# Optimization experiments

Hardware: AMD Instinct MI355X
Metric: run time of the kernel (lower is better)

## Reference

```python
import jax, jax.numpy as jnp
import numpy as np

# Dimensions: input_capsules=output_capsules=2048, slot_size=64, capsule_size=256
# slots_per_core = ceil(256/64) = 4, patch_size = (8,8) so h*w == slot_size
CI, CO, SLOT, SPC, H, W = 2048, 2048, 64, 4, 8, 8
PROBA = 0.1   # connection_probability
EPS = 1e-6    # flax nnx.LayerNorm default epsilon


def setup_inputs() -> dict:
    key = jax.random.key(0)
    k1, k2, k3 = jax.random.split(key, 3)
    x = jax.random.normal(k1, (CI, SPC, H, W), jnp.float32)
    # Wi: glorot_normal as in nnx initializers.glorot_normal()
    Wi = jax.nn.initializers.glorot_normal()(k2, (CI, SLOT, SLOT, SPC, SPC), jnp.float32)
    # LayerNorm params over the fully-flattened vector (input_capsules*capsule_size)
    ln_scale = jnp.ones((CI * SPC * SLOT,), jnp.float32)
    ln_bias = jnp.zeros((CI * SPC * SLOT,), jnp.float32)
    # Co: random sparse binary routing tensor (fast_scrramble), Bernoulli(proba)
    Co = jax.random.bernoulli(k3, PROBA, (CI, SPC, CO, SPC)).astype(jnp.float32)
    return {"x": x, "Wi": Wi, "ln_scale": ln_scale, "ln_bias": ln_bias, "Co": Co}


def reference(x, Wi, ln_scale, ln_bias, Co):
    ci, p, h, w = x.shape
    xr = x.reshape(ci, p, h * w)                      # 'ci p1 h w -> ci p1 (h w)'
    # per-capsule block matmul: 'ijklm, imk -> ilj'
    y = jnp.einsum('ijklm,imk->ilj', Wi, xr)          # (ci, spc, slot)
    y = jax.nn.gelu(y)                                # nnx.gelu (approximate tanh)
    shp = y.shape
    yf = y.reshape(-1)
    mu = jnp.mean(yf)
    var = jnp.var(yf)
    yf = (yf - mu) * jax.lax.rsqrt(var + EPS) * ln_scale + ln_bias  # global LayerNorm
    y = yf.reshape(shp)
    # sparse random-routing mixing: 'ijkl, ijm -> klm'
    out = jnp.einsum('ijkl,ijm->klm', Co, y)          # (co, spc, slot)
    return out.reshape(out.shape[0], out.shape[1], h, w)
```

## Files before the change

kernel.cpp:

```cpp
#include <hip/hip_runtime.h>
#include <hip/hip_bf16.h>

#define CI 2048
#define CO_N 2048
#define SLOT 64
#define SPC 4
#define NELEM (CI*SPC*SLOT)
#define CAP 256
#define IJ (CI*SPC)
#define S_SPLIT 8
#define NC 32

typedef __attribute__((ext_vector_type(8))) short short8;
typedef __attribute__((ext_vector_type(4))) short short4v;
typedef __attribute__((ext_vector_type(4))) float float4v;

union ABFrag { short4v h[2]; short8 v; };

__device__ __forceinline__ unsigned short f2bf(float f) {
    __hip_bfloat16 h = __float2bfloat16(f);
    return __builtin_bit_cast(unsigned short, h);
}

__device__ __forceinline__ float gelu_tanh(float x) {
    const float c0 = 0.7978845608028654f;
    float x3 = x * x * x;
    float t = tanhf(c0 * (x + 0.044715f * x3));
    return 0.5f * x * (1.0f + t);
}

__global__ __launch_bounds__(256) void k1_capsule_mm(
    const float* __restrict__ x, const float* __restrict__ Wi,
    float* __restrict__ y, float* __restrict__ psum, float* __restrict__ psumsq)
{
    __shared__ float xs[CAP];
    __shared__ float part[4][4][SLOT];
    __shared__ float ws_s[4], ws_q[4];
    const int i = blockIdx.x;
    const int t = threadIdx.x;
    xs[t] = x[(size_t)i * CAP + t];
    __syncthreads();

    const int k = t >> 2;
    const int w = t >> 6;
    const float xk0 = xs[k], xk1 = xs[64 + k], xk2 = xs[128 + k], xk3 = xs[192 + k];
    const float4* W4 = (const float4*)Wi + (size_t)i * 16384 + t;

    #pragma unroll 8
    for (int j = 0; j < SLOT; ++j) {
        float4 wv = W4[(size_t)j * 256];
        float p = wv.x * xk0 + wv.y * xk1 + wv.z * xk2 + wv.w * xk3;
        p += __shfl_xor(p, 4);
        p += __shfl_xor(p, 8);
        p += __shfl_xor(p, 16);
        p += __shfl_xor(p, 32);
        if ((t & 63) < 4) part[w][t & 63][j] = p;
    }
    __syncthreads();

    const int l2 = t >> 6, j2 = t & 63;
    float v = part[0][l2][j2] + part[1][l2][j2] + part[2][l2][j2] + part[3][l2][j2];
    float g = gelu_tanh(v);
    y[(size_t)i * CAP + t] = g;

    float s = g, q = g * g;
    #pragma unroll
    for (int off = 32; off > 0; off >>= 1) {
        s += __shfl_down(s, off);
        q += __shfl_down(q, off);
    }
    if ((t & 63) == 0) { ws_s[w] = s; ws_q[w] = q; }
    __syncthreads();
    if (t == 0) {
        psum[i]   = ws_s[0] + ws_s[1] + ws_s[2] + ws_s[3];
        psumsq[i] = ws_q[0] + ws_q[1] + ws_q[2] + ws_q[3];
    }
}

__global__ __launch_bounds__(256) void k2_stats(
    const float* __restrict__ psum, const float* __restrict__ psumsq,
    float* __restrict__ stats)
{
    __shared__ float as[4], aq[4];
    const int t = threadIdx.x;
    float s = 0.f, q = 0.f;
    for (int b = t; b < CI; b += 256) { s += psum[b]; q += psumsq[b]; }
    #pragma unroll
    for (int off = 32; off > 0; off >>= 1) {
        s += __shfl_down(s, off);
        q += __shfl_down(q, off);
    }
    if ((t & 63) == 0) { as[t >> 6] = s; aq[t >> 6] = q; }
    __syncthreads();
    if (t == 0) {
        float S = as[0] + as[1] + as[2] + as[3];
        float Q = aq[0] + aq[1] + aq[2] + aq[3];
        float mu = S / (float)NELEM;
        float var = Q / (float)NELEM - mu * mu;
        stats[0] = mu;
        stats[1] = rsqrtf(var + 1e-6f);
    }
}

__global__ __launch_bounds__(256) void k3_norm_t(
    const float* __restrict__ y, const float* __restrict__ scale,
    const float* __restrict__ bias, const float* __restrict__ stats,
    unsigned short* __restrict__ ynT)
{
    const int c = blockIdx.x;
    const int t = threadIdx.x;
    const float mu = stats[0], inv = stats[1];
    const int base = c * 2048 + t * 8;
    float4 ya = *(const float4*)(y + base);
    float4 yb = *(const float4*)(y + base + 4);
    float4 sa = *(const float4*)(scale + base);
    float4 sb = *(const float4*)(scale + base + 4);
    float4 ba = *(const float4*)(bias + base);
    float4 bb = *(const float4*)(bias + base + 4);
    const int ij = c * 32 + (t >> 3);
    const int m0 = (t & 7) * 8;
    float v[8] = { (ya.x-mu)*inv*sa.x+ba.x, (ya.y-mu)*inv*sa.y+ba.y,
                   (ya.z-mu)*inv*sa.z+ba.z, (ya.w-mu)*inv*sa.w+ba.w,
                   (yb.x-mu)*inv*sb.x+bb.x, (yb.y-mu)*inv*sb.y+bb.y,
                   (yb.z-mu)*inv*sb.z+bb.z, (yb.w-mu)*inv*sb.w+bb.w };
    #pragma unroll
    for (int e = 0; e < 8; ++e)
        ynT[(size_t)(m0 + e) * IJ + ij] = f2bf(v[e]);
}

__global__ __launch_bounds__(256) void k4_route_mfma(
    const float* __restrict__ Co, const unsigned short* __restrict__ ynT,
    float* __restrict__ out, float* __restrict__ partial, int use_partial)
{
    __shared__ unsigned short lds_a[64 * 36];
    const int t    = threadIdx.x;
    const int kb   = blockIdx.x;
    const int pc   = blockIdx.y;
    const int klb  = kb * 64;
    const int w    = t >> 6;
    const int lane = t & 63;
    const int quad = lane >> 4;
    const int n16  = lane & 15;

    const int p  = t >> 4;
    const int c4 = (t & 15) * 4;

    const float* co_base = Co + ((size_t)(pc * 1024 + 2 * p)) * IJ + klb + c4;
    const unsigned short* ynT_base = ynT + (size_t)(pc * 1024) + quad * 8;

    float4v acc[4];
    #pragma unroll
    for (int mt = 0; mt < 4; ++mt) acc[mt] = (float4v)(0.f);

    float4 co0 = *(const float4*)(co_base);
    float4 co1 = *(const float4*)(co_base + IJ);

    for (int g = 0; g < NC; ++g) {
        __syncthreads();
        unsigned int* lw = (unsigned int*)lds_a;
        lw[(c4 + 0) * 18 + p] = (unsigned int)f2bf(co0.x) | ((unsigned int)f2bf(co1.x) << 16);
        lw[(c4 + 1) * 18 + p] = (unsigned int)f2bf(co0.y) | ((unsigned int)f2bf(co1.y) << 16);
        lw[(c4 + 2) * 18 + p] = (unsigned int)f2bf(co0.z) | ((unsigned int)f2bf(co1.z) << 16);
        lw[(c4 + 3) * 18 + p] = (unsigned int)f2bf(co0.w) | ((unsigned int)f2bf(co1.w) << 16);
        __syncthreads();
        if (g + 1 < NC) {
            const float* nb = co_base + (size_t)(g + 1) * 32 * IJ;
            co0 = *(const float4*)(nb);
            co1 = *(const float4*)(nb + IJ);
        }
        const unsigned short* arow = lds_a + (w * 16 + n16) * 36 + quad * 8;
        ABFrag af;
        af.h[0] = *(const short4v*)(arow);
        af.h[1] = *(const short4v*)(arow + 4);
        const unsigned short* yb = ynT_base + (size_t)g * 32;
        #pragma unroll
        for (int mt = 0; mt < 4; ++mt) {
            short8 bf = *(const short8*)(yb + (size_t)(mt * 16 + n16) * IJ);
            acc[mt] = __builtin_amdgcn_mfma_f32_16x16x32_bf16(af.v, bf, acc[mt], 0, 0, 0);
        }
    }

    if (use_partial) {
        float* pp = partial + (size_t)pc * NELEM;
        #pragma unroll
        for (int mt = 0; mt < 4; ++mt)
            #pragma unroll
            for (int r = 0; r < 4; ++r)
                pp[(size_t)(klb + w * 16 + quad * 4 + r) * 64 + mt * 16 + n16] = acc[mt][r];
    } else {
        #pragma unroll
        for (int mt = 0; mt < 4; ++mt)
            #pragma unroll
            for (int r = 0; r < 4; ++r)
                atomicAdd(out + (size_t)(klb + w * 16 + quad * 4 + r) * 64 + mt * 16 + n16, acc[mt][r]);
    }
}

__global__ __launch_bounds__(256) void k5_reduce(
    const float* __restrict__ partial, float* __restrict__ out)
{
    const int idx = blockIdx.x * 256 + threadIdx.x;
    float s = 0.f;
    #pragma unroll
    for (int pcs = 0; pcs < S_SPLIT; ++pcs) s += partial[(size_t)pcs * NELEM + idx];
    out[idx] = s;
}

extern "C" void kernel_launch(void* const* d_in, const int* in_sizes, int n_in,
                              void* d_out, int out_size, void* d_ws, size_t ws_size,
                              hipStream_t stream) {
    const float* x        = (const float*)d_in[0];
    const float* Wi       = (const float*)d_in[1];
    const float* ln_scale = (const float*)d_in[2];
    const float* ln_bias  = (const float*)d_in[3];
    const float* Co       = (const float*)d_in[4];
    float* out = (float*)d_out;

    float* ws = (float*)d_ws;
    float* y      = ws;
    float* psum   = y + NELEM;
    float* psumsq = psum + CI;
    float* stats  = psumsq + CI;
    unsigned short* ynT = (unsigned short*)(ws + 528392);
    float* partial = ws + 790536;

    const int use_partial = (ws_size >= (size_t)(790536 + S_SPLIT * NELEM) * sizeof(float)) ? 1 : 0;

    k1_capsule_mm<<<CI, 256, 0, stream>>>(x, Wi, y, psum, psumsq);
    k2_stats<<<1, 256, 0, stream>>>(psum, psumsq, stats);
    k3_norm_t<<<256, 256, 0, stream>>>(y, ln_scale, ln_bias, stats, ynT);
    if (!use_partial)
        hipMemsetAsync(out, 0, (size_t)out_size * sizeof(float), stream);
    k4_route_mfma<<<dim3(128, S_SPLIT), 256, 0, stream>>>(Co, ynT, out, partial, use_partial);
    if (use_partial)
        k5_reduce<<<NELEM / 256, 256, 0, stream>>>(partial, out);
}
```

Before: 877.0 us.

## Fuse stats into norm kernel, restructure capsule matmul, double-buffer routing MFMA

Folds the single-block stats kernel into the normalize/transpose kernel, so every block recomputes the global mean and variance from the partial sums and one launch is removed. The capsule matmul is rewritten so each thread owns one output and loops over k with a transposed x in LDS, replacing the shuffle reductions and cross-wave combine. The routing MFMA kernel double-buffers its LDS tile, dropping one barrier per iteration, and prefetches the next B fragments into registers. Trade-offs: the Wi reads are now strided per thread (1024 floats between threads), which may hurt coalescing, and register pressure rises in the MFMA loop.

After: 873.0 us. No clear change (-0.5%).

```diff
diff --git a/kernel.cpp b/kernel.cpp
--- a/kernel.cpp
+++ b/kernel.cpp
@@ -34,34 +34,27 @@
     float* __restrict__ y, float* __restrict__ psum, float* __restrict__ psumsq)
 {
     __shared__ float xs[CAP];
-    __shared__ float part[4][4][SLOT];
     __shared__ float ws_s[4], ws_q[4];
     const int i = blockIdx.x;
     const int t = threadIdx.x;
-    xs[t] = x[(size_t)i * CAP + t];
-    __syncthreads();
-
-    const int k = t >> 2;
-    const int w = t >> 6;
-    const float xk0 = xs[k], xk1 = xs[64 + k], xk2 = xs[128 + k], xk3 = xs[192 + k];
-    const float4* W4 = (const float4*)Wi + (size_t)i * 16384 + t;
-
+    {
+        const int m = t >> 6, k = t & 63;
+        xs[k * 4 + m] = x[(size_t)i * CAP + t];
+    }
+    __syncthreads();
+
+    const int j = t >> 2;
+    const int l = t & 3;
+    const float* Wb = Wi + (size_t)i * 65536 + j * 1024 + l * 4;
+    float p = 0.f;
     #pragma unroll 8
-    for (int j = 0; j < SLOT; ++j) {
-        float4 wv = W4[(size_t)j * 256];
-        float p = wv.x * xk0 + wv.y * xk1 + wv.z * xk2 + wv.w * xk3;
-        p += __shfl_xor(p, 4);
-        p += __shfl_xor(p, 8);
-        p += __shfl_xor(p, 16);
-        p += __shfl_xor(p, 32);
-        if ((t & 63) < 4) part[w][t & 63][j] = p;
-    }
-    __syncthreads();
-
-    const int l2 = t >> 6, j2 = t & 63;
-    float v = part[0][l2][j2] + part[1][l2][j2] + part[2][l2][j2] + part[3][l2][j2];
-    float g = gelu_tanh(v);
-    y[(size_t)i * CAP + t] = g;
+    for (int k = 0; k < 64; ++k) {
+        float4 wv = *(const float4*)(Wb + k * 16);
+        float4 xv = *(const float4*)(xs + k * 4);
+        p += wv.x * xv.x + wv.y * xv.y + wv.z * xv.z + wv.w * xv.w;
+    }
+    float g = gelu_tanh(p);
+    y[(size_t)i * CAP + l * 64 + j] = g;
 
     float s = g, q = g * g;
     #pragma unroll
@@ -69,6 +62,7 @@
         s += __shfl_down(s, off);
         q += __shfl_down(q, off);
     }
+    const int w = t >> 6;
     if ((t & 63) == 0) { ws_s[w] = s; ws_q[w] = q; }
     __syncthreads();
     if (t == 0) {
@@ -77,13 +71,18 @@
     }
 }
 
-__global__ __launch_bounds__(256) void k2_stats(
-    const float* __restrict__ psum, const float* __restrict__ psumsq,
-    float* __restrict__ stats)
+__global__ __launch_bounds__(256) void k3_norm_t(
+    const float* __restrict__ y, const float* __restrict__ scale,
+    const float* __restrict__ bias, const float* __restrict__ psum,
+    const float* __restrict__ psumsq, unsigned short* __restrict__ ynT)
 {
     __shared__ float as[4], aq[4];
+    __shared__ float sh_mu, sh_inv;
+    const int c = blockIdx.x;
     const int t = threadIdx.x;
+
     float s = 0.f, q = 0.f;
+    #pragma unroll
     for (int b = t; b < CI; b += 256) { s += psum[b]; q += psumsq[b]; }
     #pragma unroll
     for (int off = 32; off > 0; off >>= 1) {
@@ -97,19 +96,12 @@
         float Q = aq[0] + aq[1] + aq[2] + aq[3];
         float mu = S / (float)NELEM;
         float var = Q / (float)NELEM - mu * mu;
-        stats[0] = mu;
-        stats[1] = rsqrtf(var + 1e-6f);
-    }
-}
-
-__global__ __launch_bounds__(256) void k3_norm_t(
-    const float* __restrict__ y, const float* __restrict__ scale,
-    const float* __restrict__ bias, const float* __restrict__ stats,
-    unsigned short* __restrict__ ynT)
-{
-    const int c = blockIdx.x;
-    const int t = threadIdx.x;
-    const float mu = stats[0], inv = stats[1];
+        sh_mu = mu;
+        sh_inv = rsqrtf(var + 1e-6f);
+    }
+    __syncthreads();
+    const float mu = sh_mu, inv = sh_inv;
+
     const int base = c * 2048 + t * 8;
     float4 ya = *(const float4*)(y + base);
     float4 yb = *(const float4*)(y + base + 4);
@@ -132,7 +124,7 @@
     const float* __restrict__ Co, const unsigned short* __restrict__ ynT,
     float* __restrict__ out, float* __restrict__ partial, int use_partial)
 {
-    __shared__ unsigned short lds_a[64 * 36];
+    __shared__ unsigned short lds_a[2][64 * 36];
     const int t    = threadIdx.x;
     const int kb   = blockIdx.x;
     const int pc   = blockIdx.y;
@@ -154,29 +146,40 @@
 
     float4 co0 = *(const float4*)(co_base);
     float4 co1 = *(const float4*)(co_base + IJ);
+    short8 bcur[4], bnxt[4];
+    #pragma unroll
+    for (int mt = 0; mt < 4; ++mt)
+        bcur[mt] = *(const short8*)(ynT_base + (size_t)(mt * 16 + n16) * IJ);
 
     for (int g = 0; g < NC; ++g) {
-        __syncthreads();
-        unsigned int* lw = (unsigned int*)lds_a;
+        unsigned int* lw = (unsigned int*)lds_a[g & 1];
         lw[(c4 + 0) * 18 + p] = (unsigned int)f2bf(co0.x) | ((unsigned int)f2bf(co1.x) << 16);
         lw[(c4 + 1) * 18 + p] = (unsigned int)f2bf(co0.y) | ((unsigned int)f2bf(co1.y) << 16);
         lw[(c4 + 2) * 18 + p] = (unsigned int)f2bf(co0.z) | ((unsigned int)f2bf(co1.z) << 16);
         lw[(c4 + 3) * 18 + p] = (unsigned int)f2bf(co0.w) | ((unsigned int)f2bf(co1.w) << 16);
         __syncthreads();
+
         if (g + 1 < NC) {
             const float* nb = co_base + (size_t)(g + 1) * 32 * IJ;
             co0 = *(const float4*)(nb);
             co1 = *(const float4*)(nb + IJ);
+            const unsigned short* yb = ynT_base + (size_t)(g + 1) * 32;
+            #pragma unroll
+            for (int mt = 0; mt < 4; ++mt)
+                bnxt[mt] = *(const short8*)(yb + (size_t)(mt * 16 + n16) * IJ);
         }
-        const unsigned short* arow = lds_a + (w * 16 + n16) * 36 + quad * 8;
+
+        const unsigned short* arow = lds_a[g & 1] + (w * 16 + n16) * 36 + quad * 8;
         ABFrag af;
         af.h[0] = *(const short4v*)(arow);
         af.h[1] = *(const short4v*)(arow + 4);
-        const unsigned short* yb = ynT_base + (size_t)g * 32;
         #pragma unroll
-        for (int mt = 0; mt < 4; ++mt) {
-            short8 bf = *(const short8*)(yb + (size_t)(mt * 16 + n16) * IJ);
-            acc[mt] = __builtin_amdgcn_mfma_f32_16x16x32_bf16(af.v, bf, acc[mt], 0, 0, 0);
+        for (int mt = 0; mt < 4; ++mt)
+            acc[mt] = __builtin_amdgcn_mfma_f32_16x16x32_bf16(af.v, bcur[mt], acc[mt], 0, 0, 0);
+
+        if (g + 1 < NC) {
+            #pragma unroll
+            for (int mt = 0; mt < 4; ++mt) bcur[mt] = bnxt[mt];
         }
     }
 
@@ -220,15 +223,13 @@
     float* y      = ws;
     float* psum   = y + NELEM;
     float* psumsq = psum + CI;
-    float* stats  = psumsq + CI;
     unsigned short* ynT = (unsigned short*)(ws + 528392);
     float* partial = ws + 790536;
 
     const int use_partial = (ws_size >= (size_t)(790536 + S_SPLIT * NELEM) * sizeof(float)) ? 1 : 0;
 
     k1_capsule_mm<<<CI, 256, 0, stream>>>(x, Wi, y, psum, psumsq);
-    k2_stats<<<1, 256, 0, stream>>>(psum, psumsq, stats);
-    k3_norm_t<<<256, 256, 0, stream>>>(y, ln_scale, ln_bias, stats, ynT);
+    k3_norm_t<<<256, 256, 0, stream>>>(y, ln_scale, ln_bias, psum, psumsq, ynT);
     if (!use_partial)
         hipMemsetAsync(out, 0, (size_t)out_size * sizeof(float), stream);
     k4_route_mfma<<<dim3(128, S_SPLIT), 256, 0, stream>>>(Co, ynT, out, partial, use_partial);
```
